# Performance work log

Measured on AMD Instinct MI355X. Metric: run time of the kernel, lower is better.

Reference implementation:

```python
import jax, jax.numpy as jnp
import numpy as np

IMG = 224; P = 16; C = 3
G = IMG // P; N = G * G            # 14, 196 patches
DIM = 768; DEPTH = 6; HEADS = 12; DH = 64; MLP = 3072
INNER = HEADS * DH                  # 768
PD = C * P * P                      # 768 patch_dim
B = 32


def _coords():
    m, n = np.meshgrid(np.arange(G), np.arange(G))
    return jnp.asarray(np.stack((m, n), axis=-1).reshape(-1, 2), jnp.float32)  # (N,2)


def _ln(x, g, b, eps=1e-5):
    mu = jnp.mean(x, -1, keepdims=True)
    var = jnp.mean((x - mu) ** 2, -1, keepdims=True)
    return (x - mu) * jax.lax.rsqrt(var + eps) * g + b


def setup_inputs() -> dict:
    key = jax.random.key(0)
    ks = jax.random.split(key, 16)
    s = 0.02
    inp = {
        "img": jax.random.normal(ks[0], (B, C, IMG, IMG), jnp.float32),
        "noise_token": jnp.zeros((1,), jnp.float32),
        "A_noise": jax.random.normal(ks[1], (B, 2, 2), jnp.float32),
        "b_noise": jax.random.normal(ks[2], (B, 2), jnp.float32),
        "A_mean": jnp.eye(2, dtype=jnp.float32),
        "b_mean": jnp.zeros((2,), jnp.float32),
        "A_std": jnp.zeros((2, 2), jnp.float32),   # variance_init=0.0
        "b_std": jnp.zeros((2,), jnp.float32),
        "band_width": jnp.asarray(1.0, jnp.float32),
        "Wp": jax.random.normal(ks[3], (PD, DIM), jnp.float32) * s,
        "bp": jnp.zeros((DIM,), jnp.float32),
        "ln1_g": jnp.ones((DEPTH, DIM), jnp.float32),
        "ln1_b": jnp.zeros((DEPTH, DIM), jnp.float32),
        "Wqkv": jax.random.normal(ks[4], (DEPTH, DIM, 3 * INNER), jnp.float32) * s,
        "Wout": jax.random.normal(ks[5], (DEPTH, INNER, DIM), jnp.float32) * s,
        "bout": jnp.zeros((DEPTH, DIM), jnp.float32),
        "ln2_g": jnp.ones((DEPTH, DIM), jnp.float32),
        "ln2_b": jnp.zeros((DEPTH, DIM), jnp.float32),
        "Wff1": jax.random.normal(ks[6], (DEPTH, DIM, MLP), jnp.float32) * s,
        "bff1": jnp.zeros((DEPTH, MLP), jnp.float32),
        "Wff2": jax.random.normal(ks[7], (DEPTH, MLP, DIM), jnp.float32) * s,
        "bff2": jnp.zeros((DEPTH, DIM), jnp.float32),
        "Wep": jax.random.normal(ks[8], (DIM, PD), jnp.float32) * s,
        "bep": jnp.zeros((PD,), jnp.float32),
    }
    return inp


def reference(img, noise_token, A_noise, b_noise, A_mean, b_mean, A_std, b_std,
              band_width, Wp, bp, ln1_g, ln1_b, Wqkv, Wout, bout,
              ln2_g, ln2_b, Wff1, bff1, Wff2, bff2, Wep, bep):
    del noise_token  # deleted in the original forward
    b = img.shape[0]
    X = _coords()  # (N,2) base patch grid coords, non-trainable buffer
    # patchify: b c (h p1) (w p2) -> b (h w) (p1 p2 c)
    x = img.reshape(b, C, G, P, G, P).transpose(0, 2, 4, 3, 5, 1).reshape(b, N, PD)
    x = x @ Wp + bp
    # stochastic affine transform of coordinates
    A = A_mean + jax.nn.softplus(A_std) * A_noise          # (b,2,2)
    bt = b_mean + jax.nn.softplus(b_std) * b_noise         # (b,2)
    Xt = jnp.einsum('pd,bdo->bpo', X, A) + bt[:, None, :]  # (b,N,2)
    # RBF attention scores: dots[b,i,j] = -||Xt[b,j] - X[i]||^2 / band_width
    diff = Xt[:, None, :, :] - X[None, :, None, :]         # (b,N,N,2)
    dots = -jnp.sum(diff ** 2, axis=-1) / band_width       # (b,N,N)
    attn = jax.nn.softmax(dots, axis=-1)                   # same for all heads/layers
    for l in range(DEPTH):
        y = _ln(x, ln1_g[l], ln1_b[l])
        qkv = y @ Wqkv[l]                                  # q,k unused (pos_only=True)
        v = qkv[..., 2 * INNER:].reshape(b, N, HEADS, DH).transpose(0, 2, 1, 3)
        o = jnp.einsum('bij,bhjd->bhid', attn, v)
        o = o.transpose(0, 2, 1, 3).reshape(b, N, INNER)
        x = o @ Wout[l] + bout[l]                          # NOTE: no residual on attention (matches source)
        h = _ln(x, ln2_g[l], ln2_b[l])
        h = jax.nn.gelu(h @ Wff1[l] + bff1[l], approximate=False) @ Wff2[l] + bff2[l]
        x = x + h
    x = x @ Wep + bep
    # un-patchify: b (h w) (p1 p2 c) -> b c (h p1) (w p2)
    out = x.reshape(b, G, G, P, P, C).transpose(0, 5, 1, 3, 2, 4).reshape(b, C, IMG, IMG)
    return out
```

## Files before the change

### kernel.cpp

```cpp
#include <hip/hip_runtime.h>
#include <hip/hip_bf16.h>
#include <math.h>

#define NTOK 196
#define KPAD 224
#define BATCH 32
#define ROWS (BATCH * NTOK)
#define DIMC 768
#define MLPD 3072

typedef __hip_bfloat16 bf16;
typedef short bf16x8 __attribute__((ext_vector_type(8)));
typedef float f32x4 __attribute__((ext_vector_type(4)));

__device__ __forceinline__ void gload16(const void* g, void* l) {
    __builtin_amdgcn_global_load_lds(
        (__attribute__((address_space(1))) void*)const_cast<void*>(g),
        (__attribute__((address_space(3))) void*)l, 16, 0, 0);
}

__device__ __forceinline__ float softplus_f(float x) {
    return fmaxf(x, 0.f) + log1pf(expf(-fabsf(x)));
}
__device__ __forceinline__ float gelu_f(float x) {
    return 0.5f * x * (1.f + erff(x * 0.70710678118654752f));
}
__device__ __forceinline__ float to_f(float x) { return x; }
__device__ __forceinline__ float to_f(bf16 x) { return __bfloat162float(x); }

__global__ __launch_bounds__(64) void attn_kernel(
    const float* __restrict__ A_noise, const float* __restrict__ b_noise,
    const float* __restrict__ A_mean,  const float* __restrict__ b_mean,
    const float* __restrict__ A_std,   const float* __restrict__ b_std,
    const float* __restrict__ bwp, bf16* __restrict__ attn)
{
    int bi = blockIdx.x;
    int b = bi / NTOK, i = bi % NTOK;
    int lane = threadIdx.x;
    float A00 = A_mean[0] + softplus_f(A_std[0]) * A_noise[b * 4 + 0];
    float A01 = A_mean[1] + softplus_f(A_std[1]) * A_noise[b * 4 + 1];
    float A10 = A_mean[2] + softplus_f(A_std[2]) * A_noise[b * 4 + 2];
    float A11 = A_mean[3] + softplus_f(A_std[3]) * A_noise[b * 4 + 3];
    float bt0 = b_mean[0] + softplus_f(b_std[0]) * b_noise[b * 2 + 0];
    float bt1 = b_mean[1] + softplus_f(b_std[1]) * b_noise[b * 2 + 1];
    float inv_bw = 1.f / bwp[0];
    float Xi0 = (float)(i % 14), Xi1 = (float)(i / 14);
    float d[4];
    float mx = -1e30f;
    #pragma unroll
    for (int r = 0; r < 4; ++r) {
        int j = lane + r * 64;
        if (j < NTOK) {
            float Xj0 = (float)(j % 14), Xj1 = (float)(j / 14);
            float t0 = Xj0 * A00 + Xj1 * A10 + bt0 - Xi0;
            float t1 = Xj0 * A01 + Xj1 * A11 + bt1 - Xi1;
            d[r] = -(t0 * t0 + t1 * t1) * inv_bw;
            mx = fmaxf(mx, d[r]);
        } else d[r] = -1e30f;
    }
    for (int off = 1; off < 64; off <<= 1) mx = fmaxf(mx, __shfl_xor(mx, off));
    float e[4]; float s = 0.f;
    #pragma unroll
    for (int r = 0; r < 4; ++r) {
        int j = lane + r * 64;
        e[r] = (j < NTOK) ? expf(d[r] - mx) : 0.f;
        s += e[r];
    }
    for (int off = 1; off < 64; off <<= 1) s += __shfl_xor(s, off);
    float inv = 1.f / s;
    bf16* row = attn + (long)bi * KPAD;
    #pragma unroll
    for (int r = 0; r < 4; ++r) {
        int j = lane + r * 64;
        if (j < KPAD) row[j] = __float2bfloat16(j < NTOK ? e[r] * inv : 0.f);
    }
}

__global__ __launch_bounds__(256) void patchify_kernel(
    const float* __restrict__ img, bf16* __restrict__ Xp)
{
    long idx = (long)blockIdx.x * 256 + threadIdx.x;
    if (idx >= (long)ROWS * DIMC) return;
    int pd = (int)(idx % DIMC); long r = idx / DIMC;
    int n = (int)(r % NTOK); int b = (int)(r / NTOK);
    int c = pd % 3; int pp = pd / 3; int p2 = pp % 16; int p1 = pp / 16;
    int gw = n % 14, gh = n / 14;
    int h = gh * 16 + p1, w = gw * 16 + p2;
    Xp[idx] = __float2bfloat16(img[(((long)b * 3 + c) * 224 + h) * 224 + w]);
}

__global__ __launch_bounds__(256) void unpatchify_kernel(
    const float* __restrict__ xe, float* __restrict__ out)
{
    long idx = (long)blockIdx.x * 256 + threadIdx.x;
    if (idx >= (long)BATCH * 3 * 224 * 224) return;
    int w = (int)(idx % 224); long r = idx / 224;
    int h = (int)(r % 224); r /= 224;
    int c = (int)(r % 3); int b = (int)(r / 3);
    int gh = h / 16, p1 = h % 16, gw = w / 16, p2 = w % 16;
    int n = gh * 14 + gw;
    int pd = (p1 * 16 + p2) * 3 + c;
    out[idx] = xe[((long)b * NTOK + n) * DIMC + pd];
}

__global__ __launch_bounds__(256) void ln_kernel(
    const float* __restrict__ x, const float* __restrict__ g,
    const float* __restrict__ bb, bf16* __restrict__ y)
{
    int row = blockIdx.x;
    const float* xr = x + (long)row * DIMC;
    bf16* yr = y + (long)row * DIMC;
    int t = threadIdx.x;
    float v0 = xr[t], v1 = xr[t + 256], v2 = xr[t + 512];
    float s = v0 + v1 + v2;
    float s2 = v0 * v0 + v1 * v1 + v2 * v2;
    for (int off = 32; off; off >>= 1) { s += __shfl_down(s, off); s2 += __shfl_down(s2, off); }
    __shared__ float ps[4], ps2[4];
    if ((t & 63) == 0) { ps[t >> 6] = s; ps2[t >> 6] = s2; }
    __syncthreads();
    float S = ps[0] + ps[1] + ps[2] + ps[3];
    float S2 = ps2[0] + ps2[1] + ps2[2] + ps2[3];
    float mean = S * (1.f / DIMC);
    float var = S2 * (1.f / DIMC) - mean * mean;
    float rs = rsqrtf(var + 1e-5f);
    yr[t]       = __float2bfloat16((v0 - mean) * rs * g[t]       + bb[t]);
    yr[t + 256] = __float2bfloat16((v1 - mean) * rs * g[t + 256] + bb[t + 256]);
    yr[t + 512] = __float2bfloat16((v2 - mean) * rs * g[t + 512] + bb[t + 512]);
}

template<typename TIN>
__global__ __launch_bounds__(256) void transpose_cvt(
    const TIN* __restrict__ in, bf16* __restrict__ out,
    int R, int C, int ldin, int ldout, int Rpad, long sIn, long sOut)
{
    __shared__ float tile[32][33];
    in  += (long)blockIdx.z * sIn;
    out += (long)blockIdx.z * sOut;
    int c0 = blockIdx.x * 32, r0 = blockIdx.y * 32;
    int tx = threadIdx.x & 31, ty = threadIdx.x >> 5;
    #pragma unroll
    for (int i = 0; i < 32; i += 8) {
        int r = r0 + ty + i, c = c0 + tx;
        float v = 0.f;
        if (r < R && c < C) v = to_f(in[(long)r * ldin + c]);
        tile[ty + i][tx] = v;
    }
    __syncthreads();
    #pragma unroll
    for (int i = 0; i < 32; i += 8) {
        int c = c0 + ty + i, r = r0 + tx;
        if (c < C && r < Rpad) out[(long)c * ldout + r] = __float2bfloat16(tile[tx][ty + i]);
    }
}

__global__ __launch_bounds__(256) void cvt_kernel(const float* __restrict__ in,
                                                  bf16* __restrict__ out, int n)
{
    int i = blockIdx.x * 256 + threadIdx.x;
    if (i < n) out[i] = __float2bfloat16(in[i]);
}

__global__ __launch_bounds__(256) void cvt_wv_kernel(const float* __restrict__ Wqkv,
                                                     bf16* __restrict__ out)
{
    long i = (long)blockIdx.x * 256 + threadIdx.x;
    if (i >= 6L * 768 * 768) return;
    int c = (int)(i % 768); long rl = i / 768;
    int r = (int)(rl % 768); int l = (int)(rl / 768);
    out[i] = __float2bfloat16(Wqkv[((long)l * 768 + r) * 2304 + 1536 + c]);
}

template<int BN, int ACT, int ACCUM, int OUTF32, int GUARDM>
__global__ __launch_bounds__(256) void gemm_bf16(
    const bf16* __restrict__ A, const bf16* __restrict__ Bt,
    const float* __restrict__ bias, void* __restrict__ Cv,
    int M, int K, int lda, int ldb, int ldc,
    long sA, long sB, long sC)
{
    constexpr int FN = BN / 32;
    constexpr int LPT = 2 + BN / 64;
    constexpr int BSTRIDE = BN * 32;
    constexpr int SMEM = (BN == 128) ? 49152 : 36864;
    __shared__ __align__(16) char smem[SMEM];
    bf16* As = (bf16*)smem;
    bf16* Bs = (bf16*)(smem + 3 * 8192);
    A  += (long)blockIdx.z * sA;
    Bt += (long)blockIdx.z * sB;
    const int m0 = blockIdx.y * 128, n0 = blockIdx.x * BN;
    const int t = threadIdx.x, wave = t >> 6, lane = t & 63;
    const int lrow = t >> 2, lcol = (t & 3) * 8;
    const bf16* ag = A  + (long)(m0 + lrow) * lda + lcol;
    const bf16* bg = Bt + (long)(n0 + lrow) * ldb + lcol;
    const int fr = lane & 15, kq = lane >> 4;
    const int wr = wave >> 1, wc = wave & 1;
    f32x4 acc[4][FN];
    #pragma unroll
    for (int m = 0; m < 4; ++m)
        #pragma unroll
        for (int n = 0; n < FN; ++n) acc[m][n] = (f32x4){0.f, 0.f, 0.f, 0.f};

    auto stage = [&](int kt, int bufi) {
        const int k0 = kt << 5;
        bf16* ab = As + bufi * 4096 + wave * 512;
        bf16* bb = Bs + bufi * BSTRIDE + wave * 512;
        gload16(ag + k0, ab);
        gload16(ag + 64 * (long)lda + k0, ab + 2048);
        gload16(bg + k0, bb);
        if constexpr (BN == 128) gload16(bg + 64 * (long)ldb + k0, bb + 2048);
    };
    auto compute = [&](int bufi) {
        const bf16* as = As + bufi * 4096;
        const bf16* bs = Bs + bufi * BSTRIDE;
        bf16x8 af[4], bfv[FN];
        #pragma unroll
        for (int m = 0; m < 4; ++m)
            af[m] = *(const bf16x8*)&as[(wr * 64 + m * 16 + fr) * 32 + kq * 8];
        #pragma unroll
        for (int n = 0; n < FN; ++n)
            bfv[n] = *(const bf16x8*)&bs[(wc * (BN / 2) + n * 16 + fr) * 32 + kq * 8];
        __builtin_amdgcn_s_setprio(1);
        #pragma unroll
        for (int m = 0; m < 4; ++m)
            #pragma unroll
            for (int n = 0; n < FN; ++n)
                acc[m][n] = __builtin_amdgcn_mfma_f32_16x16x32_bf16(af[m], bfv[n], acc[m][n], 0, 0, 0);
        __builtin_amdgcn_s_setprio(0);
    };

    const int nt = K >> 5;
    stage(0, 0);
    stage(1, 1);
    int cur = 0, pf = 2;
    for (int it = 0; it < nt - 1; ++it) {
        asm volatile("s_waitcnt vmcnt(%0)" :: "n"(LPT) : "memory");
        __builtin_amdgcn_s_barrier();
        __builtin_amdgcn_sched_barrier(0);
        if (it + 2 < nt) stage(it + 2, pf);
        compute(cur);
        cur = (cur == 2) ? 0 : cur + 1;
        pf  = (pf  == 2) ? 0 : pf + 1;
    }
    asm volatile("s_waitcnt vmcnt(0)" ::: "memory");
    __builtin_amdgcn_s_barrier();
    __builtin_amdgcn_sched_barrier(0);
    compute(cur);
    __syncthreads();

    const int rbase = kq * 4;
    if constexpr (OUTF32) {
        static_assert(BN == 64, "f32 epilogue assumes BN=64");
        float* Cs = (float*)smem;
        #pragma unroll
        for (int n = 0; n < FN; ++n) {
            int lc = wc * (BN / 2) + n * 16 + fr;
            float bi = bias ? bias[n0 + lc] : 0.f;
            #pragma unroll
            for (int m = 0; m < 4; ++m)
                #pragma unroll
                for (int r = 0; r < 4; ++r) {
                    int lr = wr * 64 + m * 16 + rbase + r;
                    float vv = acc[m][n][r] + bi;
                    if (ACT) vv = gelu_f(vv);
                    Cs[lr * BN + lc] = vv;
                }
        }
        __syncthreads();
        float* Cp = (float*)Cv + (long)blockIdx.z * sC;
        #pragma unroll
        for (int i = 0; i < (128 * BN) / (256 * 4); ++i) {
            int chunk = i * 256 + t;
            int row = chunk / (BN / 4), c4 = (chunk % (BN / 4)) * 4;
            int gm = m0 + row;
            if (GUARDM && gm >= M) continue;
            float4 v4 = *(const float4*)&Cs[row * BN + c4];
            float* p = Cp + (long)gm * ldc + n0 + c4;
            if (ACCUM) {
                float4 o4 = *(const float4*)p;
                v4.x += o4.x; v4.y += o4.y; v4.z += o4.z; v4.w += o4.w;
            }
            *(float4*)p = v4;
        }
    } else {
        bf16* Cs = (bf16*)smem;
        #pragma unroll
        for (int n = 0; n < FN; ++n) {
            int lc = wc * (BN / 2) + n * 16 + fr;
            float bi = bias ? bias[n0 + lc] : 0.f;
            #pragma unroll
            for (int m = 0; m < 4; ++m)
                #pragma unroll
                for (int r = 0; r < 4; ++r) {
                    int lr = wr * 64 + m * 16 + rbase + r;
                    float vv = acc[m][n][r] + bi;
                    if (ACT) vv = gelu_f(vv);
                    Cs[lr * BN + lc] = __float2bfloat16(vv);
                }
        }
        __syncthreads();
        bf16* Cp = (bf16*)Cv + (long)blockIdx.z * sC;
        #pragma unroll
        for (int i = 0; i < (128 * BN) / (256 * 8); ++i) {
            int chunk = i * 256 + t;
            int row = chunk / (BN / 8), c8 = (chunk % (BN / 8)) * 8;
            int gm = m0 + row;
            if (GUARDM && gm >= M) continue;
            *(bf16x8*)(Cp + (long)gm * ldc + n0 + c8) = *(const bf16x8*)&Cs[row * BN + c8];
        }
    }
}

extern "C" void kernel_launch(void* const* d_in, const int* in_sizes, int n_in,
                              void* d_out, int out_size, void* d_ws, size_t ws_size,
                              hipStream_t stream) {
    const float* img     = (const float*)d_in[0];
    const float* A_noise = (const float*)d_in[2];
    const float* b_noise = (const float*)d_in[3];
    const float* A_mean  = (const float*)d_in[4];
    const float* b_mean  = (const float*)d_in[5];
    const float* A_std   = (const float*)d_in[6];
    const float* b_std   = (const float*)d_in[7];
    const float* band_w  = (const float*)d_in[8];
    const float* Wp      = (const float*)d_in[9];
    const float* bp      = (const float*)d_in[10];
    const float* ln1_g   = (const float*)d_in[11];
    const float* ln1_b   = (const float*)d_in[12];
    const float* Wqkv    = (const float*)d_in[13];
    const float* Wout    = (const float*)d_in[14];
    const float* bout    = (const float*)d_in[15];
    const float* ln2_g   = (const float*)d_in[16];
    const float* ln2_b   = (const float*)d_in[17];
    const float* Wff1    = (const float*)d_in[18];
    const float* bff1    = (const float*)d_in[19];
    const float* Wff2    = (const float*)d_in[20];
    const float* bff2    = (const float*)d_in[21];
    const float* Wep     = (const float*)d_in[22];
    const float* bep     = (const float*)d_in[23];
    float* out = (float*)d_out;

    char* w = (char*)d_ws;
    bf16* WpT  = (bf16*)w; w += 768L * 768 * 2;
    bf16* WepT = (bf16*)w; w += 768L * 768 * 2;
    bf16* WvoT = (bf16*)w; w += 6L * 768 * 768 * 2;
    bf16* Wf1T = (bf16*)w; w += 6L * 3072 * 768 * 2;
    bf16* Wf2T = (bf16*)w; w += 6L * 768 * 3072 * 2;
    bf16* attnb = (bf16*)w; w += (long)(ROWS + 64) * KPAD * 2;
    bf16* Xpb  = (bf16*)w; w += (long)ROWS * DIMC * 2;
    bf16* yb   = (bf16*)w; w += (long)ROWS * DIMC * 2;
    bf16* yTb  = (bf16*)w; w += (long)BATCH * DIMC * KPAD * 2;
    bf16* ya   = (bf16*)w; w += (long)ROWS * DIMC * 2;
    bf16* h1b  = (bf16*)w; w += (long)ROWS * MLPD * 2;
    float* x   = (float*)w; w += (long)ROWS * DIMC * 4;
    bf16* WoT  = h1b;
    bf16* Wvb  = h1b + 6L * 768 * 768;

    transpose_cvt<float><<<dim3(24, 24, 1), 256, 0, stream>>>(Wp,  WpT,  768, 768, 768, 768, 768, 0, 0);
    transpose_cvt<float><<<dim3(24, 24, 1), 256, 0, stream>>>(Wep, WepT, 768, 768, 768, 768, 768, 0, 0);
    transpose_cvt<float><<<dim3(24, 24, 6), 256, 0, stream>>>(Wout, WoT, 768, 768, 768, 768, 768,
                                                              768L * 768, 768L * 768);
    cvt_wv_kernel<<<(int)((6L * 768 * 768 + 255) / 256), 256, 0, stream>>>(Wqkv, Wvb);
    transpose_cvt<float><<<dim3(96, 24, 6), 256, 0, stream>>>(Wff1, Wf1T, 768, 3072, 3072, 768, 768,
                                                              768L * 3072, 3072L * 768);
    transpose_cvt<float><<<dim3(24, 96, 6), 256, 0, stream>>>(Wff2, Wf2T, 3072, 768, 768, 3072, 3072,
                                                              3072L * 768, 768L * 3072);
    gemm_bf16<64, 0, 0, 0, 0><<<dim3(12, 6, 6), 256, 0, stream>>>(
        WoT, Wvb, nullptr, WvoT, 768, 768, 768, 768, 768,
        768L * 768, 768L * 768, 768L * 768);

    attn_kernel<<<ROWS, 64, 0, stream>>>(A_noise, b_noise, A_mean, b_mean, A_std, b_std, band_w, attnb);

    patchify_kernel<<<(ROWS * DIMC + 255) / 256, 256, 0, stream>>>(img, Xpb);
    gemm_bf16<64, 0, 0, 1, 0><<<dim3(12, 49, 1), 256, 0, stream>>>(
        Xpb, WpT, bp, x, ROWS, 768, 768, 768, 768, 0, 0, 0);

    for (int l = 0; l < 6; ++l) {
        ln_kernel<<<ROWS, 256, 0, stream>>>(x, ln1_g + l * 768, ln1_b + l * 768, yb);
        transpose_cvt<bf16><<<dim3(24, 7, 32), 256, 0, stream>>>(
            yb, yTb, NTOK, 768, 768, KPAD, KPAD, (long)NTOK * 768, (long)768 * KPAD);
        gemm_bf16<64, 0, 0, 0, 1><<<dim3(12, 2, BATCH), 256, 0, stream>>>(
            attnb, yTb, nullptr, ya, NTOK, KPAD, KPAD, KPAD, 768,
            (long)NTOK * KPAD, (long)768 * KPAD, (long)NTOK * 768);
        gemm_bf16<64, 0, 0, 1, 0><<<dim3(12, 49, 1), 256, 0, stream>>>(
            ya, WvoT + (long)l * 768 * 768, bout + l * 768, x, ROWS, 768, 768, 768, 768, 0, 0, 0);
        ln_kernel<<<ROWS, 256, 0, stream>>>(x, ln2_g + l * 768, ln2_b + l * 768, yb);
        gemm_bf16<128, 1, 0, 0, 0><<<dim3(24, 49, 1), 256, 0, stream>>>(
            yb, Wf1T + (long)l * 3072 * 768, bff1 + l * 3072, h1b, ROWS, 768, 768, 768, 3072, 0, 0, 0);
        gemm_bf16<64, 0, 1, 1, 0><<<dim3(12, 49, 1), 256, 0, stream>>>(
            h1b, Wf2T + (long)l * 768 * 3072, bff2 + l * 768, x, ROWS, 3072, 3072, 3072, 768, 0, 0, 0);
    }

    bf16* xb = Xpb;
    float* xe = (float*)h1b;
    cvt_kernel<<<(ROWS * DIMC + 255) / 256, 256, 0, stream>>>(x, xb, ROWS * DIMC);
    gemm_bf16<64, 0, 0, 1, 0><<<dim3(12, 49, 1), 256, 0, stream>>>(
        xb, WepT, bep, xe, ROWS, 768, 768, 768, 768, 0, 0, 0);
    unpatchify_kernel<<<(BATCH * 3 * 224 * 224 + 255) / 256, 256, 0, stream>>>(xe, out);
}
```

Before: 1.239 ms.

## Use 256x256 tile GEMM for MLP, split-K FF2 with fused residual+LayerNorm

Adds a 512-thread 256x256-tile bf16 MFMA GEMM with double-buffered direct-to-LDS loads, swizzled LDS and priority hints, and uses it for the FF1 (with GELU) and FF2 GEMMs. FF2 is split-K in two and writes fp32 partials. A new combine kernel sums the partials, bias and residual and applies the next layer's LN1, replacing the separate ln and cvt kernels. The goal is better data reuse and MFMA utilisation on the dominant MLP GEMMs and fewer launches. In exchange it adds partial-sum buffers, 128KB of LDS per block and more tile padding on M (25×256 rows).

```diff
diff --git a/kernel.cpp b/kernel.cpp
--- a/kernel.cpp
+++ b/kernel.cpp
@@ -128,6 +128,45 @@
     yr[t + 512] = __float2bfloat16((v2 - mean) * rs * g[t + 512] + bb[t + 512]);
 }
 
+template<int MODE>
+__global__ __launch_bounds__(256) void combine_ln(
+    const float* __restrict__ P0, const float* __restrict__ P1,
+    const float* __restrict__ bias, float* __restrict__ x,
+    const float* __restrict__ g, const float* __restrict__ bb,
+    bf16* __restrict__ zb)
+{
+    int row = blockIdx.x;
+    float* xr = x + (long)row * DIMC;
+    const float* p0 = P0 + (long)row * DIMC;
+    const float* p1 = P1 + (long)row * DIMC;
+    bf16* zr = zb + (long)row * DIMC;
+    int t = threadIdx.x;
+    float v0 = xr[t]       + p0[t]       + p1[t]       + bias[t];
+    float v1 = xr[t + 256] + p0[t + 256] + p1[t + 256] + bias[t + 256];
+    float v2 = xr[t + 512] + p0[t + 512] + p1[t + 512] + bias[t + 512];
+    xr[t] = v0; xr[t + 256] = v1; xr[t + 512] = v2;
+    if (MODE == 1) {
+        zr[t]       = __float2bfloat16(v0);
+        zr[t + 256] = __float2bfloat16(v1);
+        zr[t + 512] = __float2bfloat16(v2);
+        return;
+    }
+    float s = v0 + v1 + v2;
+    float s2 = v0 * v0 + v1 * v1 + v2 * v2;
+    for (int off = 32; off; off >>= 1) { s += __shfl_down(s, off); s2 += __shfl_down(s2, off); }
+    __shared__ float ps[4], ps2[4];
+    if ((t & 63) == 0) { ps[t >> 6] = s; ps2[t >> 6] = s2; }
+    __syncthreads();
+    float S = ps[0] + ps[1] + ps[2] + ps[3];
+    float S2 = ps2[0] + ps2[1] + ps2[2] + ps2[3];
+    float mean = S * (1.f / DIMC);
+    float var = S2 * (1.f / DIMC) - mean * mean;
+    float rs = rsqrtf(var + 1e-5f);
+    zr[t]       = __float2bfloat16((v0 - mean) * rs * g[t]       + bb[t]);
+    zr[t + 256] = __float2bfloat16((v1 - mean) * rs * g[t + 256] + bb[t + 256]);
+    zr[t + 512] = __float2bfloat16((v2 - mean) * rs * g[t + 512] + bb[t + 512]);
+}
+
 template<typename TIN>
 __global__ __launch_bounds__(256) void transpose_cvt(
     const TIN* __restrict__ in, bf16* __restrict__ out,
@@ -151,13 +190,6 @@
         int c = c0 + ty + i, r = r0 + tx;
         if (c < C && r < Rpad) out[(long)c * ldout + r] = __float2bfloat16(tile[tx][ty + i]);
     }
-}
-
-__global__ __launch_bounds__(256) void cvt_kernel(const float* __restrict__ in,
-                                                  bf16* __restrict__ out, int n)
-{
-    int i = blockIdx.x * 256 + threadIdx.x;
-    if (i < n) out[i] = __float2bfloat16(in[i]);
 }
 
 __global__ __launch_bounds__(256) void cvt_wv_kernel(const float* __restrict__ Wqkv,
@@ -305,6 +337,173 @@
             int gm = m0 + row;
             if (GUARDM && gm >= M) continue;
             *(bf16x8*)(Cp + (long)gm * ldc + n0 + c8) = *(const bf16x8*)&Cs[row * BN + c8];
+        }
+    }
+}
+
+#define MFMA16(MO)                                                             \
+    _Pragma("unroll")                                                          \
+    for (int mm = 0; mm < 4; ++mm) {                                           \
+        _Pragma("unroll")                                                      \
+        for (int nf = 0; nf < 4; ++nf)                                         \
+            acc[(MO) + mm][nf] = __builtin_amdgcn_mfma_f32_16x16x32_bf16(      \
+                av[mm], bfv[nf], acc[(MO) + mm][nf], 0, 0, 0);                 \
+    }
+#define LDA8(b_, ks_, mf_) (*(const bf16x8*)(Ab + (b_) * 32768 + (ks_) * 16384 + rdA + (mf_) * 1024))
+#define LDB8(b_, ks_, nf_) (*(const bf16x8*)(Bb + (b_) * 32768 + (ks_) * 16384 + rdB + (nf_) * 1024))
+
+template<int EPI>
+__global__ __launch_bounds__(512, 2) void gemm256(
+    const bf16* __restrict__ A, const bf16* __restrict__ Bt,
+    const float* __restrict__ bias, void* __restrict__ Cv,
+    int M, int K, int lda, int ldb, int ldc, long kOffZ, long sCz)
+{
+    extern __shared__ char smem[];
+    A  += (long)blockIdx.z * kOffZ;
+    Bt += (long)blockIdx.z * kOffZ;
+    const int m0 = blockIdx.y * 256, n0 = blockIdx.x * 256;
+    const int t = threadIdx.x, wave = t >> 6, lane = t & 63;
+    const int wm = wave >> 2, wn = wave & 3;
+    const int fr = lane & 15, kq = lane >> 4;
+    const int swz = (fr >> 1) & 3;
+    const int r0 = t >> 2;
+    const int cS = (t & 3) ^ ((r0 >> 1) & 3);
+    char* Ab = smem;
+    char* Bb = smem + 65536;
+    const int rdA = (wm * 128 + fr) * 64 + ((kq ^ swz) << 4);
+    const int rdB = (wn * 64 + fr) * 64 + ((kq ^ swz) << 4);
+
+    f32x4 acc[8][4];
+    #pragma unroll
+    for (int m = 0; m < 8; ++m)
+        #pragma unroll
+        for (int n = 0; n < 4; ++n) acc[m][n] = (f32x4){0.f, 0.f, 0.f, 0.f};
+
+    const bf16* aSrc = A  + (long)(m0 + r0) * lda + cS * 8;
+    const bf16* bSrc = Bt + (long)(n0 + r0) * ldb + cS * 8;
+    auto stA = [&](int kt, int ks, int bufi) {
+        const bf16* s = aSrc + kt * 64 + ks * 32;
+        char* d = Ab + bufi * 32768 + ks * 16384 + t * 16;
+        gload16(s, d);
+        gload16(s + 128L * lda, d + 8192);
+    };
+    auto stB = [&](int kt, int ks, int bufi) {
+        const bf16* s = bSrc + kt * 64 + ks * 32;
+        char* d = Bb + bufi * 32768 + ks * 16384 + t * 16;
+        gload16(s, d);
+        gload16(s + 128L * ldb, d + 8192);
+    };
+
+    const int NT = K >> 6;
+    stA(0, 0, 0); stB(0, 0, 0); stA(0, 1, 0); stB(0, 1, 0);
+    asm volatile("s_waitcnt vmcnt(4)" ::: "memory");
+    __builtin_amdgcn_s_barrier();
+
+    bf16x8 av[4], bfv[4];
+    for (int it = 0; it < NT; ++it) {
+        const int b = it & 1, nb = b ^ 1;
+        const bool pre = (it + 1 < NT);
+        #pragma unroll
+        for (int nf = 0; nf < 4; ++nf) bfv[nf] = LDB8(b, 0, nf);
+        #pragma unroll
+        for (int mm = 0; mm < 4; ++mm) av[mm] = LDA8(b, 0, mm);
+        if (pre) stA(it + 1, 0, nb);
+        __builtin_amdgcn_s_barrier();
+        asm volatile("s_waitcnt lgkmcnt(0)" ::: "memory");
+        __builtin_amdgcn_sched_barrier(0);
+        __builtin_amdgcn_s_setprio(1);
+        MFMA16(0);
+        __builtin_amdgcn_s_setprio(0);
+        __builtin_amdgcn_s_barrier();
+        #pragma unroll
+        for (int mm = 0; mm < 4; ++mm) av[mm] = LDA8(b, 0, 4 + mm);
+        if (pre) stB(it + 1, 0, nb);
+        __builtin_amdgcn_s_barrier();
+        asm volatile("s_waitcnt lgkmcnt(0)" ::: "memory");
+        __builtin_amdgcn_sched_barrier(0);
+        __builtin_amdgcn_s_setprio(1);
+        MFMA16(4);
+        __builtin_amdgcn_s_setprio(0);
+        if (pre) { asm volatile("s_waitcnt vmcnt(4)" ::: "memory"); }
+        else     { asm volatile("s_waitcnt vmcnt(0)" ::: "memory"); }
+        __builtin_amdgcn_s_barrier();
+        #pragma unroll
+        for (int nf = 0; nf < 4; ++nf) bfv[nf] = LDB8(b, 1, nf);
+        #pragma unroll
+        for (int mm = 0; mm < 4; ++mm) av[mm] = LDA8(b, 1, mm);
+        if (pre) stA(it + 1, 1, nb);
+        __builtin_amdgcn_s_barrier();
+        asm volatile("s_waitcnt lgkmcnt(0)" ::: "memory");
+        __builtin_amdgcn_sched_barrier(0);
+        __builtin_amdgcn_s_setprio(1);
+        MFMA16(0);
+        __builtin_amdgcn_s_setprio(0);
+        __builtin_amdgcn_s_barrier();
+        #pragma unroll
+        for (int mm = 0; mm < 4; ++mm) av[mm] = LDA8(b, 1, 4 + mm);
+        if (pre) stB(it + 1, 1, nb);
+        __builtin_amdgcn_s_barrier();
+        asm volatile("s_waitcnt lgkmcnt(0)" ::: "memory");
+        __builtin_amdgcn_sched_barrier(0);
+        __builtin_amdgcn_s_setprio(1);
+        MFMA16(4);
+        __builtin_amdgcn_s_setprio(0);
+        if (pre) { asm volatile("s_waitcnt vmcnt(4)" ::: "memory"); }
+        else     { asm volatile("s_waitcnt vmcnt(0)" ::: "memory"); }
+        __builtin_amdgcn_s_barrier();
+    }
+
+    __syncthreads();
+    const int colb = wn * 64 + fr;
+    if constexpr (EPI == 0) {
+        bf16* Cs = (bf16*)smem;
+        float bsv[4];
+        #pragma unroll
+        for (int nf = 0; nf < 4; ++nf) bsv[nf] = bias[n0 + colb + nf * 16];
+        #pragma unroll
+        for (int mf = 0; mf < 8; ++mf)
+            #pragma unroll
+            for (int nf = 0; nf < 4; ++nf)
+                #pragma unroll
+                for (int r = 0; r < 4; ++r) {
+                    int row = wm * 128 + mf * 16 + kq * 4 + r;
+                    float vv = gelu_f(acc[mf][nf][r] + bsv[nf]);
+                    Cs[row * 256 + colb + nf * 16] = __float2bfloat16(vv);
+                }
+        __syncthreads();
+        bf16* Cp = (bf16*)Cv;
+        #pragma unroll
+        for (int i = 0; i < 16; ++i) {
+            int chunk = i * 512 + t;
+            int row = chunk >> 5, c = (chunk & 31) * 8;
+            int gm = m0 + row;
+            if (gm < M)
+                *(bf16x8*)(Cp + (long)gm * ldc + n0 + c) = *(const bf16x8*)&Cs[row * 256 + c];
+        }
+    } else {
+        float* Cs = (float*)smem;
+        float* Cp = (float*)Cv + (long)blockIdx.z * sCz;
+        #pragma unroll
+        for (int h = 0; h < 2; ++h) {
+            if (h) __syncthreads();
+            if (wm == h) {
+                #pragma unroll
+                for (int mf = 0; mf < 8; ++mf)
+                    #pragma unroll
+                    for (int nf = 0; nf < 4; ++nf)
+                        #pragma unroll
+                        for (int r = 0; r < 4; ++r)
+                            Cs[(mf * 16 + kq * 4 + r) * 256 + colb + nf * 16] = acc[mf][nf][r];
+            }
+            __syncthreads();
+            #pragma unroll
+            for (int i = 0; i < 16; ++i) {
+                int chunk = i * 512 + t;
+                int row = chunk >> 6, c4 = (chunk & 63) * 4;
+                int gm = m0 + h * 128 + row;
+                if (gm < M)
+                    *(float4*)(Cp + (long)gm * ldc + n0 + c4) = *(const float4*)&Cs[row * 256 + c4];
+            }
         }
     }
 }
@@ -350,8 +549,12 @@
     bf16* ya   = (bf16*)w; w += (long)ROWS * DIMC * 2;
     bf16* h1b  = (bf16*)w; w += (long)ROWS * MLPD * 2;
     float* x   = (float*)w; w += (long)ROWS * DIMC * 4;
-    bf16* WoT  = h1b;
-    bf16* Wvb  = h1b + 6L * 768 * 768;
+    float* P0 = (float*)Xpb;
+    float* P1 = P0 + (long)ROWS * DIMC;
+    bf16* WoT = h1b;
+    bf16* Wvb = h1b + 6L * 768 * 768;
+    bf16* zb  = h1b;
+    float* xe = (float*)((char*)h1b + (long)ROWS * DIMC * 2);
 
     transpose_cvt<float><<<dim3(24, 24, 1), 256, 0, stream>>>(Wp,  WpT,  768, 768, 768, 768, 768, 0, 0);
     transpose_cvt<float><<<dim3(24, 24, 1), 256, 0, stream>>>(Wep, WepT, 768, 768, 768, 768, 768, 0, 0);
@@ -371,27 +574,32 @@
     patchify_kernel<<<(ROWS * DIMC + 255) / 256, 256, 0, stream>>>(img, Xpb);
     gemm_bf16<64, 0, 0, 1, 0><<<dim3(12, 49, 1), 256, 0, stream>>>(
         Xpb, WpT, bp, x, ROWS, 768, 768, 768, 768, 0, 0, 0);
+    ln_kernel<<<ROWS, 256, 0, stream>>>(x, ln1_g, ln1_b, zb);
 
     for (int l = 0; l < 6; ++l) {
-        ln_kernel<<<ROWS, 256, 0, stream>>>(x, ln1_g + l * 768, ln1_b + l * 768, yb);
         transpose_cvt<bf16><<<dim3(24, 7, 32), 256, 0, stream>>>(
-            yb, yTb, NTOK, 768, 768, KPAD, KPAD, (long)NTOK * 768, (long)768 * KPAD);
+            zb, yTb, NTOK, 768, 768, KPAD, KPAD, (long)NTOK * 768, (long)768 * KPAD);
         gemm_bf16<64, 0, 0, 0, 1><<<dim3(12, 2, BATCH), 256, 0, stream>>>(
             attnb, yTb, nullptr, ya, NTOK, KPAD, KPAD, KPAD, 768,
             (long)NTOK * KPAD, (long)768 * KPAD, (long)NTOK * 768);
         gemm_bf16<64, 0, 0, 1, 0><<<dim3(12, 49, 1), 256, 0, stream>>>(
             ya, WvoT + (long)l * 768 * 768, bout + l * 768, x, ROWS, 768, 768, 768, 768, 0, 0, 0);
         ln_kernel<<<ROWS, 256, 0, stream>>>(x, ln2_g + l * 768, ln2_b + l * 768, yb);
-        gemm_bf16<128, 1, 0, 0, 0><<<dim3(24, 49, 1), 256, 0, stream>>>(
-            yb, Wf1T + (long)l * 3072 * 768, bff1 + l * 3072, h1b, ROWS, 768, 768, 768, 3072, 0, 0, 0);
-        gemm_bf16<64, 0, 1, 1, 0><<<dim3(12, 49, 1), 256, 0, stream>>>(
-            h1b, Wf2T + (long)l * 768 * 3072, bff2 + l * 768, x, ROWS, 3072, 3072, 3072, 768, 0, 0, 0);
-    }
-
-    bf16* xb = Xpb;
-    float* xe = (float*)h1b;
-    cvt_kernel<<<(ROWS * DIMC + 255) / 256, 256, 0, stream>>>(x, xb, ROWS * DIMC);
+        gemm256<0><<<dim3(12, 25, 1), 512, 131072, stream>>>(
+            yb, Wf1T + (long)l * 3072 * 768, bff1 + l * 3072, h1b,
+            ROWS, 768, 768, 768, 3072, 0, 0);
+        gemm256<1><<<dim3(3, 25, 2), 512, 131072, stream>>>(
+            h1b, Wf2T + (long)l * 768 * 3072, nullptr, P0,
+            ROWS, 1536, 3072, 3072, 768, 1536, (long)ROWS * DIMC);
+        if (l < 5)
+            combine_ln<0><<<ROWS, 256, 0, stream>>>(P0, P1, bff2 + l * 768, x,
+                ln1_g + (l + 1) * 768, ln1_b + (l + 1) * 768, zb);
+        else
+            combine_ln<1><<<ROWS, 256, 0, stream>>>(P0, P1, bff2 + l * 768, x,
+                ln1_g, ln1_b, zb);
+    }
+
     gemm_bf16<64, 0, 0, 1, 0><<<dim3(12, 49, 1), 256, 0, stream>>>(
-        xb, WepT, bep, xe, ROWS, 768, 768, 768, 768, 0, 0, 0);
+        zb, WepT, bep, xe, ROWS, 768, 768, 768, 768, 0, 0, 0);
     unpatchify_kernel<<<(BATCH * 3 * 224 * 224 + 255) / 256, 256, 0, stream>>>(xe, out);
 }
```

After: 1.363 ms. 10.0% more time.
